# Kernel optimization log

Hardware: AMD Instinct MI355X
Metric: run time of the kernel (lower is better)

Reference implementation:

```python
import jax, jax.numpy as jnp
import numpy as np
from jax import lax

SPARSE_TH = 0.01
STRIDE = (1, 1)


def setup_inputs() -> dict:
    key = jax.random.key(0)
    k1, k2, k3 = jax.random.split(key, 3)
    x = jax.random.normal(k1, (32, 56, 56, 256), dtype=jnp.float32)  # NHWC
    # weight: (out_channels, in_channels, kh, kw); scale so a fraction falls below sparse_th
    weight = jax.random.normal(k2, (256, 256, 3, 3), dtype=jnp.float32) * 0.05
    bias = jax.random.normal(k3, (256,), dtype=jnp.float32)
    return {"x": x, "weight": weight, "bias": bias}


def reference(x, weight, bias):
    # Threshold weights: |w| < sparse_th -> 0 (the sparse kernel computes the
    # identical math as a dense valid conv with the masked weight)
    w = jnp.where(jnp.abs(weight) < SPARSE_TH, jnp.zeros_like(weight), weight)
    # OIHW -> HWIO for NHWC conv
    w_hwio = jnp.transpose(w, (2, 3, 1, 0))
    out = lax.conv_general_dilated(
        x, w_hwio,
        window_strides=STRIDE,
        padding="VALID",
        dimension_numbers=("NHWC", "HWIO", "NHWC"),
    )
    return out + bias.reshape(1, 1, 1, -1)
```

## Files before the change

### kernel.cpp

```cpp
#include <hip/hip_runtime.h>
#include <hip/hip_bf16.h>


typedef __bf16 bf16x8 __attribute__((ext_vector_type(8)));
typedef float f32x4 __attribute__((ext_vector_type(4)));

#define GLOBAL_AS __attribute__((address_space(1)))
#define LDS_AS __attribute__((address_space(3)))

static __device__ __forceinline__ void glds16(const void* g, void* l) {
    __builtin_amdgcn_global_load_lds((const GLOBAL_AS unsigned int*)g,
                                     (LDS_AS unsigned int*)l, 16, 0, 0);
}

static __device__ __forceinline__ unsigned short f2bf(float f) {
    unsigned int u = __float_as_uint(f);
    unsigned int r = u + 0x7FFFu + ((u >> 16) & 1u);
    return (unsigned short)(r >> 16);
}

__global__ void cvt_xw(const float* __restrict__ x, unsigned short* __restrict__ xb,
                       const float* __restrict__ w, unsigned short* __restrict__ wt) {
    const int NXB = 32 * 56 * 56 * 256 / (256 * 8);
    if (blockIdx.x < NXB) {
        int i = (blockIdx.x * 256 + threadIdx.x) * 8;
        const float4* p = (const float4*)(x + i);
        float4 a = p[0], b = p[1];
        uint4 v;
        v.x = (unsigned)f2bf(a.x) | ((unsigned)f2bf(a.y) << 16);
        v.y = (unsigned)f2bf(a.z) | ((unsigned)f2bf(a.w) << 16);
        v.z = (unsigned)f2bf(b.x) | ((unsigned)f2bf(b.y) << 16);
        v.w = (unsigned)f2bf(b.z) | ((unsigned)f2bf(b.w) << 16);
        *(uint4*)(xb + i) = v;
    } else {
        int co = blockIdx.x - NXB;
        int ci = threadIdx.x;
        const float* src = w + co * 2304 + ci * 9;
        unsigned short* dst = wt + co * 2304 + ci;
#pragma unroll
        for (int khw = 0; khw < 9; ++khw) {
            float v = src[khw];
            v = (fabsf(v) < 0.01f) ? 0.0f : v;
            dst[khw * 256] = f2bf(v);
        }
    }
}

static __device__ __forceinline__ int swz_key(int row16) {
    return (row16 & 3) ^ ((row16 >> 2) & 3);
}

__global__ __launch_bounds__(256) void conv_gemm(
    const unsigned short* __restrict__ Xb,
    const unsigned short* __restrict__ Wt,
    const float* __restrict__ bias,
    float* __restrict__ Out)
{
    __shared__ __align__(16) unsigned short As[2][128 * 32];
    __shared__ __align__(16) unsigned short Bs[2][128 * 32];

    const int tid  = threadIdx.x;
    const int lane = tid & 63;
    const int wave = tid >> 6;

    const int bx = blockIdx.x;
    const int xcd = bx & 7;
    const int slt = bx >> 3;
    const int v   = xcd * 182 + (xcd < 2 ? xcd : 2) + slt;
    const int m0  = (v >> 1) * 128;
    const int co0 = (v & 1) * 128;

    const int srow = lane >> 2;
    const int schunk_g = (lane & 3) ^ swz_key(srow);
    const int scol = schunk_g * 8;

    const unsigned short* a_src[2];
    const unsigned short* b_src[2];
#pragma unroll
    for (int r = 0; r < 2; ++r) {
        int row = r * 64 + wave * 16 + srow;
        int m = m0 + row;
        int n = m / 2916;
        int rem = m - n * 2916;
        int oh = rem / 54;
        int ow = rem - oh * 54;
        a_src[r] = Xb + (((n * 56 + oh) * 56 + ow) << 8) + scol;
        b_src[r] = Wt + (co0 + row) * 2304 + scol;
    }

    const int fm = lane & 15;
    const int fq = lane >> 4;
    const int wm = (wave >> 1) * 64;
    const int wn = (wave & 1) * 64;
    const int slot8 = (fq ^ swz_key(fm)) * 8;

    f32x4 acc[4][4];
#pragma unroll
    for (int i = 0; i < 4; ++i)
#pragma unroll
        for (int j = 0; j < 4; ++j)
            acc[i][j] = (f32x4){0.f, 0.f, 0.f, 0.f};

#pragma unroll
    for (int r = 0; r < 2; ++r) {
        glds16(a_src[r], &As[0][wave * 512 + r * 2048]);
        glds16(b_src[r], &Bs[0][wave * 512 + r * 2048]);
    }

#pragma unroll 1
    for (int kc = 0; kc < 72; ++kc) {
        __syncthreads();

        if (kc < 71) {
            const int kcn = kc + 1;
            const int khwn = kcn >> 3;
            const int khn = (khwn * 11) >> 5;
            const int kwn = khwn - khn * 3;
            const int aoffn = ((khn * 56 + kwn) << 8) + (kcn & 7) * 32;
            const int boffn = kcn * 32;
            const int b = kcn & 1;
#pragma unroll
            for (int r = 0; r < 2; ++r) {
                glds16(a_src[r] + aoffn, &As[b][wave * 512 + r * 2048]);
                glds16(b_src[r] + boffn, &Bs[b][wave * 512 + r * 2048]);
            }
        }

        const unsigned short* Ab = As[kc & 1];
        const unsigned short* Bb = Bs[kc & 1];
        bf16x8 af[4], bfr[4];
#pragma unroll
        for (int mi = 0; mi < 4; ++mi)
            af[mi] = *(const bf16x8*)&Ab[(wm + mi * 16 + fm) * 32 + slot8];
#pragma unroll
        for (int ni = 0; ni < 4; ++ni)
            bfr[ni] = *(const bf16x8*)&Bb[(wn + ni * 16 + fm) * 32 + slot8];
#pragma unroll
        for (int mi = 0; mi < 4; ++mi)
#pragma unroll
            for (int ni = 0; ni < 4; ++ni)
                acc[mi][ni] = __builtin_amdgcn_mfma_f32_16x16x32_bf16(
                    af[mi], bfr[ni], acc[mi][ni], 0, 0, 0);
    }

    float bv[4];
#pragma unroll
    for (int ni = 0; ni < 4; ++ni) bv[ni] = bias[co0 + wn + ni * 16 + fm];
#pragma unroll
    for (int mi = 0; mi < 4; ++mi) {
#pragma unroll
        for (int reg = 0; reg < 4; ++reg) {
            int m = m0 + wm + mi * 16 + fq * 4 + reg;
            float* orow = Out + m * 256 + co0 + wn + fm;
#pragma unroll
            for (int ni = 0; ni < 4; ++ni)
                orow[ni * 16] = acc[mi][ni][reg] + bv[ni];
        }
    }
}

extern "C" void kernel_launch(void* const* d_in, const int* in_sizes, int n_in,
                              void* d_out, int out_size, void* d_ws, size_t ws_size,
                              hipStream_t stream) {
    const float* x    = (const float*)d_in[0];
    const float* w    = (const float*)d_in[1];
    const float* bias = (const float*)d_in[2];
    float* out = (float*)d_out;

    const int NX = 32 * 56 * 56 * 256;
    unsigned short* xb = (unsigned short*)d_ws;
    unsigned short* wt = xb + NX;

    cvt_xw<<<NX / (256 * 8) + 256, 256, 0, stream>>>(x, xb, w, wt);
    conv_gemm<<<729 * 2, 256, 0, stream>>>(xb, wt, bias, out);
}
```

Measured before the change: 302.5 us.

## Load weight fragments directly to registers, drop B LDS staging, unroll K by two

Weight (B) tiles are no longer staged through shared memory. Each lane now loads its MFMA B fragments straight from global memory into registers, double-buffered across a K loop unrolled by two. This halves LDS usage and removes the B LDS reads and writes, and launch bounds now request 3 blocks per CU to raise occupancy. In exchange, each wave reloads weights from global/L2 without sharing them across waves, and the loads are uncoalesced 16-byte reads spread across rows 2304 elements apart.

```diff
diff --git a/kernel.cpp b/kernel.cpp
--- a/kernel.cpp
+++ b/kernel.cpp
@@ -46,24 +46,30 @@
     }
 }
 
-static __device__ __forceinline__ int swz_key(int row16) {
-    return (row16 & 3) ^ ((row16 >> 2) & 3);
+static __device__ __forceinline__ int swz_key(int r) {
+    return (r & 3) ^ ((r >> 2) & 3);
 }
 
-__global__ __launch_bounds__(256) void conv_gemm(
+static __device__ __forceinline__ int a_off(int kcn) {
+    int khw = kcn >> 3;
+    int kh = (khw * 11) >> 5;
+    int kw = khw - kh * 3;
+    return ((kh * 56 + kw) << 8) + (kcn & 7) * 32;
+}
+
+__global__ __launch_bounds__(256, 3) void conv_gemm(
     const unsigned short* __restrict__ Xb,
     const unsigned short* __restrict__ Wt,
     const float* __restrict__ bias,
     float* __restrict__ Out)
 {
     __shared__ __align__(16) unsigned short As[2][128 * 32];
-    __shared__ __align__(16) unsigned short Bs[2][128 * 32];
 
     const int tid  = threadIdx.x;
     const int lane = tid & 63;
     const int wave = tid >> 6;
 
-    const int bx = blockIdx.x;
+    const int bx  = blockIdx.x;
     const int xcd = bx & 7;
     const int slt = bx >> 3;
     const int v   = xcd * 182 + (xcd < 2 ? xcd : 2) + slt;
@@ -71,11 +77,9 @@
     const int co0 = (v & 1) * 128;
 
     const int srow = lane >> 2;
-    const int schunk_g = (lane & 3) ^ swz_key(srow);
-    const int scol = schunk_g * 8;
+    const int scol = ((lane & 3) ^ swz_key(srow)) * 8;
 
     const unsigned short* a_src[2];
-    const unsigned short* b_src[2];
 #pragma unroll
     for (int r = 0; r < 2; ++r) {
         int row = r * 64 + wave * 16 + srow;
@@ -85,7 +89,6 @@
         int oh = rem / 54;
         int ow = rem - oh * 54;
         a_src[r] = Xb + (((n * 56 + oh) * 56 + ow) << 8) + scol;
-        b_src[r] = Wt + (co0 + row) * 2304 + scol;
     }
 
     const int fm = lane & 15;
@@ -93,6 +96,8 @@
     const int wm = (wave >> 1) * 64;
     const int wn = (wave & 1) * 64;
     const int slot8 = (fq ^ swz_key(fm)) * 8;
+
+    const unsigned short* b_lane = Wt + (co0 + wn + fm) * 2304 + fq * 8;
 
     f32x4 acc[4][4];
 #pragma unroll
@@ -102,45 +107,62 @@
             acc[i][j] = (f32x4){0.f, 0.f, 0.f, 0.f};
 
 #pragma unroll
-    for (int r = 0; r < 2; ++r) {
+    for (int r = 0; r < 2; ++r)
         glds16(a_src[r], &As[0][wave * 512 + r * 2048]);
-        glds16(b_src[r], &Bs[0][wave * 512 + r * 2048]);
-    }
+    bf16x8 b0[4], b1[4];
+#pragma unroll
+    for (int ni = 0; ni < 4; ++ni)
+        b0[ni] = *(const bf16x8*)(b_lane + ni * 16 * 2304);
 
 #pragma unroll 1
-    for (int kc = 0; kc < 72; ++kc) {
+    for (int kc = 0; kc < 72; kc += 2) {
         __syncthreads();
-
-        if (kc < 71) {
+        {
             const int kcn = kc + 1;
-            const int khwn = kcn >> 3;
-            const int khn = (khwn * 11) >> 5;
-            const int kwn = khwn - khn * 3;
-            const int aoffn = ((khn * 56 + kwn) << 8) + (kcn & 7) * 32;
-            const int boffn = kcn * 32;
-            const int b = kcn & 1;
+            const int ao = a_off(kcn), bo = kcn * 32;
 #pragma unroll
-            for (int r = 0; r < 2; ++r) {
-                glds16(a_src[r] + aoffn, &As[b][wave * 512 + r * 2048]);
-                glds16(b_src[r] + boffn, &Bs[b][wave * 512 + r * 2048]);
-            }
+            for (int r = 0; r < 2; ++r)
+                glds16(a_src[r] + ao, &As[1][wave * 512 + r * 2048]);
+#pragma unroll
+            for (int ni = 0; ni < 4; ++ni)
+                b1[ni] = *(const bf16x8*)(b_lane + ni * 16 * 2304 + bo);
+        }
+        {
+            bf16x8 af[4];
+#pragma unroll
+            for (int mi = 0; mi < 4; ++mi)
+                af[mi] = *(const bf16x8*)&As[0][(wm + mi * 16 + fm) * 32 + slot8];
+#pragma unroll
+            for (int mi = 0; mi < 4; ++mi)
+#pragma unroll
+                for (int ni = 0; ni < 4; ++ni)
+                    acc[mi][ni] = __builtin_amdgcn_mfma_f32_16x16x32_bf16(
+                        af[mi], b0[ni], acc[mi][ni], 0, 0, 0);
         }
 
-        const unsigned short* Ab = As[kc & 1];
-        const unsigned short* Bb = Bs[kc & 1];
-        bf16x8 af[4], bfr[4];
+        __syncthreads();
+        if (kc + 2 < 72) {
+            const int kcn = kc + 2;
+            const int ao = a_off(kcn), bo = kcn * 32;
 #pragma unroll
-        for (int mi = 0; mi < 4; ++mi)
-            af[mi] = *(const bf16x8*)&Ab[(wm + mi * 16 + fm) * 32 + slot8];
-#pragma unroll
-        for (int ni = 0; ni < 4; ++ni)
-            bfr[ni] = *(const bf16x8*)&Bb[(wn + ni * 16 + fm) * 32 + slot8];
-#pragma unroll
-        for (int mi = 0; mi < 4; ++mi)
+            for (int r = 0; r < 2; ++r)
+                glds16(a_src[r] + ao, &As[0][wave * 512 + r * 2048]);
 #pragma unroll
             for (int ni = 0; ni < 4; ++ni)
-                acc[mi][ni] = __builtin_amdgcn_mfma_f32_16x16x32_bf16(
-                    af[mi], bfr[ni], acc[mi][ni], 0, 0, 0);
+                b0[ni] = *(const bf16x8*)(b_lane + ni * 16 * 2304 + bo);
+        }
+        {
+            bf16x8 af[4];
+#pragma unroll
+            for (int mi = 0; mi < 4; ++mi)
+                af[mi] = *(const bf16x8*)&As[1][(wm + mi * 16 + fm) * 32 + slot8];
+#pragma unroll
+            for (int mi = 0; mi < 4; ++mi)
+#pragma unroll
+                for (int ni = 0; ni < 4; ++ni)
+                    acc[mi][ni] = __builtin_amdgcn_mfma_f32_16x16x32_bf16(
+                        af[mi], b1[ni], acc[mi][ni], 0, 0, 0);
+        }
     }
 
     float bv[4];
```

New measurement: 410.7 us. 35.7% more time.
